# Optimization experiments

Hardware: AMD Instinct MI355X
Metric: run time of the kernel (lower is better)

The kernel has to match this reference:

```python
import jax, jax.numpy as jnp
import numpy as np

N_NODES = 50000
N_EDGES = 800000
N_GRAPHS = 64
IN_DIM, HID_DIM, OUT_DIM = 128, 256, 1


def setup_inputs() -> dict:
    key = jax.random.key(0)
    ks = jax.random.split(key, 9)
    x = jax.random.normal(ks[0], (N_NODES, IN_DIM), dtype=jnp.float32)
    edge_index = jax.random.randint(ks[1], (2, N_EDGES), 0, N_NODES, dtype=jnp.int64)
    batch = jnp.sort(jax.random.randint(ks[2], (N_NODES,), 0, N_GRAPHS, dtype=jnp.int64))
    W1 = jax.random.normal(ks[3], (IN_DIM, HID_DIM), dtype=jnp.float32) / np.sqrt(IN_DIM)
    b1 = jax.random.normal(ks[4], (HID_DIM,), dtype=jnp.float32) * 0.01
    W2 = jax.random.normal(ks[5], (HID_DIM, HID_DIM), dtype=jnp.float32) / np.sqrt(HID_DIM)
    b2 = jax.random.normal(ks[6], (HID_DIM,), dtype=jnp.float32) * 0.01
    Wfc = jax.random.normal(ks[7], (HID_DIM, OUT_DIM), dtype=jnp.float32) / np.sqrt(HID_DIM)
    bfc = jax.random.normal(ks[8], (OUT_DIM,), dtype=jnp.float32) * 0.01
    return {"x": x, "edge_index": edge_index, "batch": batch,
            "W1": W1, "b1": b1, "W2": W2, "b2": b2, "Wfc": Wfc, "bfc": bfc}


def reference(x, edge_index, batch, W1, b1, W2, b2, Wfc, bfc):
    N = x.shape[0]
    loop = jnp.arange(N, dtype=edge_index.dtype)
    src = jnp.concatenate([edge_index[0], loop])  # [E+N] message sources
    dst = jnp.concatenate([edge_index[1], loop])  # [E+N] aggregation targets
    # symmetric GCN normalization with self-loops
    deg = jax.ops.segment_sum(jnp.ones_like(dst, dtype=x.dtype), dst, num_segments=N)
    dinv = jnp.where(deg > 0, jax.lax.rsqrt(deg), 0.0)
    norm = (dinv[src] * dinv[dst])[:, None]  # [E+N, 1]

    def gcn(h, W, b):
        h = h @ W                                     # [N, H]
        msg = h[src] * norm                           # gather + scale
        return jax.ops.segment_sum(msg, dst, num_segments=N) + b

    h = jax.nn.relu(gcn(x, W1, b1))
    h = jax.nn.relu(gcn(h, W2, b2))
    # global mean pool over graphs in the batch
    counts = jax.ops.segment_sum(jnp.ones((N,), dtype=h.dtype), batch, num_segments=N_GRAPHS)
    sums = jax.ops.segment_sum(h, batch, num_segments=N_GRAPHS)
    pooled = sums / jnp.maximum(counts, 1.0)[:, None]  # [G, H]
    out = pooled @ Wfc + bfc                           # [G, 1]
    return out.squeeze(-1)
```

## Files before the change

### kernel.cpp

```cpp
#include <hip/hip_runtime.h>
#include <hip/hip_bf16.h>

#define N_NODES 50000
#define N_EDGES 800000
#define N_GRAPHS 64
#define IN_DIM 128
#define HID_DIM 256
#define M_PAD 50048

typedef short sh8 __attribute__((ext_vector_type(8)));
typedef float f4 __attribute__((ext_vector_type(4)));
typedef float f2 __attribute__((ext_vector_type(2)));
typedef unsigned short us4 __attribute__((ext_vector_type(4)));

__device__ __forceinline__ unsigned short bf16rne(float f) {
    unsigned int u = __float_as_uint(f);
    return (unsigned short)((u + 0x7FFFu + ((u >> 16) & 1u)) >> 16);
}
__device__ __forceinline__ float bf2f(unsigned short b) {
    return __uint_as_float((unsigned int)b << 16);
}
__device__ __forceinline__ unsigned char f32_to_fp8(float v) {
    int p = __builtin_amdgcn_cvt_pk_fp8_f32(v, v, 0, false);
    return (unsigned char)(p & 0xFF);
}

__device__ __forceinline__ void gl2lds16(const unsigned short* g, unsigned short* l) {
    __builtin_amdgcn_global_load_lds(
        (const __attribute__((address_space(1))) void*)g,
        (__attribute__((address_space(3))) void*)l, 16, 0, 0);
}


__device__ __forceinline__ void wconv_one(const float* __restrict__ W,
                                          unsigned short* __restrict__ Bh, int i) {
    int k = i >> 8, c = i & 255;
    size_t pos = (size_t)(k >> 5) * 8192 + (size_t)(((c >> 4) * 4 + ((k >> 3) & 3)) * 128 + (c & 15) * 8 + (k & 7));
    Bh[pos] = bf16rne(W[i]);
}

__global__ __launch_bounds__(256)
void k_prep(const float* __restrict__ W1, unsigned short* __restrict__ Bh1,
            const float* __restrict__ W2, unsigned short* __restrict__ Bh2,
            const int* __restrict__ batch, int* __restrict__ bounds, float* __restrict__ sums,
            const int* __restrict__ dst, int* __restrict__ deg_i) {
    const int T = gridDim.x * 256;
    const int gid = blockIdx.x * 256 + threadIdx.x;
    for (int i = gid; i < IN_DIM * 256; i += T) wconv_one(W1, Bh1, i);
    for (int i = gid; i < HID_DIM * 256; i += T) wconv_one(W2, Bh2, i);
    for (int i = gid; i < N_GRAPHS * HID_DIM; i += T) sums[i] = 0.f;
    if (gid <= N_GRAPHS) {
        int lo = 0, hi = N_NODES;
        while (lo < hi) {
            int mid = (lo + hi) >> 1;
            if (batch[mid] < gid) lo = mid + 1; else hi = mid;
        }
        bounds[gid] = lo;
    }
    for (int e = gid; e < N_EDGES; e += T) atomicAdd(&deg_i[dst[e]], 1);
}

#define SCAN_BLK 1024
#define SCAN_NBLK ((N_NODES + SCAN_BLK - 1) / SCAN_BLK)

__global__ __launch_bounds__(SCAN_BLK)
void k_scan_blk(const int* __restrict__ deg, int* __restrict__ row_start,
                float* __restrict__ dinv, int* __restrict__ blk_tot) {
    __shared__ int tmp[SCAN_BLK];
    int t = threadIdx.x;
    int i = blockIdx.x * SCAN_BLK + t;
    int d = 0;
    if (i < N_NODES) {
        d = deg[i];
        dinv[i] = rsqrtf((float)d + 1.0f);
    }
    tmp[t] = d;
    __syncthreads();
    #pragma unroll
    for (int off = 1; off < SCAN_BLK; off <<= 1) {
        int v = (t >= off) ? tmp[t - off] : 0;
        __syncthreads();
        tmp[t] += v;
        __syncthreads();
    }
    if (i < N_NODES) row_start[i] = tmp[t] - d;
    if (t == SCAN_BLK - 1) blk_tot[blockIdx.x] = tmp[t];
}

__global__ __launch_bounds__(SCAN_BLK)
void k_scan_add(int* __restrict__ row_start, const int* __restrict__ blk_tot) {
    __shared__ int soff;
    int t = threadIdx.x;
    int bid = blockIdx.x;
    if (t < 64) {
        int v = (t < bid) ? blk_tot[t] : 0;
        #pragma unroll
        for (int m = 1; m < 64; m <<= 1) v += __shfl_xor(v, m, 64);
        if (t == 0) soff = v;
    }
    __syncthreads();
    int i = bid * SCAN_BLK + t;
    if (i < N_NODES) row_start[i] += soff;
    if (bid == 0 && t == 0) row_start[N_NODES] = N_EDGES;
}

__global__ __launch_bounds__(256)
void k_x2f8(const float* __restrict__ x, const float* __restrict__ dinv,
            unsigned char* __restrict__ xf8) {
    int i = blockIdx.x * blockDim.x + threadIdx.x;
    if (i >= N_NODES * IN_DIM / 4) return;
    float4 v = ((const float4*)x)[i];
    float s = dinv[i >> 5] * 8.f;
    unsigned int lo = (unsigned int)__builtin_amdgcn_cvt_pk_fp8_f32(v.x * s, v.y * s, 0, false) & 0xFFFFu;
    unsigned int hi = (unsigned int)__builtin_amdgcn_cvt_pk_fp8_f32(v.z * s, v.w * s, 0, false) & 0xFFFFu;
    ((unsigned int*)xf8)[i] = lo | (hi << 16);
}

__global__ void k_csr_fill(const int* __restrict__ src, const int* __restrict__ dst,
                           const int* __restrict__ row_start, int* __restrict__ cursor,
                           int* __restrict__ col) {
    int e = blockIdx.x * blockDim.x + threadIdx.x;
    if (e < N_EDGES) {
        int d = dst[e];
        int pos = atomicAdd(&cursor[d], 1);
        col[row_start[d] + pos] = src[e];
    }
}


template<int MODE>
__global__ __launch_bounds__(256)
void k_gemm_mfma(const unsigned short* __restrict__ Ah,
                 const unsigned short* __restrict__ Bh,
                 const float* __restrict__ dinv, const float* __restrict__ bias,
                 unsigned short* __restrict__ Cbf, unsigned char* __restrict__ Cf8,
                 int M, int K) {
    __shared__ unsigned short AhL[2][2][2048];

    const int tid = threadIdx.x;
    const int wv = tid >> 6, lane = tid & 63;
    const int m0 = blockIdx.x * 64;

    const int ar = wv * 16 + (lane & 15);
    const int kseg = lane >> 4;
    const unsigned short* aph = Ah + (size_t)(m0 + ar) * K + kseg * 8;
    const int adoff = (wv * 64 + lane) * 8;

    f4 acc[4][4];
    #pragma unroll
    for (int mi = 0; mi < 4; ++mi)
        #pragma unroll
        for (int nj = 0; nj < 4; ++nj)
            acc[mi][nj] = f4{0.f, 0.f, 0.f, 0.f};

    const int nsteps = K >> 6;
    gl2lds16(aph, &AhL[0][0][adoff]);
    gl2lds16(aph + 32, &AhL[0][1][adoff]);

    int cur = 0;
    for (int s = 0; s < nsteps; ++s) {
        __syncthreads();
        if (s + 1 < nsteps) {
            gl2lds16(aph + (s + 1) * 64, &AhL[cur ^ 1][0][adoff]);
            gl2lds16(aph + (s + 1) * 64 + 32, &AhL[cur ^ 1][1][adoff]);
        }
        #pragma unroll
        for (int kk = 0; kk < 2; ++kk) {
            const int bstep = s * 2 + kk;
            const unsigned short* gb = Bh + (size_t)bstep * 8192 + wv * 2048 + lane * 8;
            sh8 bfh[4];
            #pragma unroll
            for (int nj = 0; nj < 4; ++nj)
                bfh[nj] = *reinterpret_cast<const sh8*>(gb + nj * 512);
            sh8 afh[4];
            #pragma unroll
            for (int mi = 0; mi < 4; ++mi)
                afh[mi] = *reinterpret_cast<const sh8*>(&AhL[cur][kk][mi * 512 + lane * 8]);
            #pragma unroll
            for (int mi = 0; mi < 4; ++mi)
                #pragma unroll
                for (int nj = 0; nj < 4; ++nj)
                    acc[mi][nj] = __builtin_amdgcn_mfma_f32_16x16x32_bf16(afh[mi], bfh[nj], acc[mi][nj], 0, 0, 0);
        }
        cur ^= 1;
    }

    #pragma unroll
    for (int mi = 0; mi < 4; ++mi) {
        #pragma unroll
        for (int q = 0; q < 4; ++q) {
            int grow = m0 + mi * 16 + (lane >> 4) * 4 + q;
            if (grow < M) {
                float dm16 = (MODE == 0) ? dinv[grow] * 16.f : 0.f;
                #pragma unroll
                for (int nj = 0; nj < 4; ++nj) {
                    int gcol = wv * 64 + nj * 16 + (lane & 15);
                    float v = acc[mi][nj][q];
                    if (MODE == 0) {
                        Cf8[(size_t)grow * 256 + gcol] = f32_to_fp8(v * dm16);
                    } else {
                        Cbf[(size_t)grow * 256 + gcol] = bf16rne(fmaxf(v + bias[gcol], 0.f));
                    }
                }
            }
        }
    }
}


__global__ __launch_bounds__(256)
void k_agg_x(const float* __restrict__ x, const unsigned char* __restrict__ xf8,
             const int* __restrict__ row_start, const int* __restrict__ col,
             const float* __restrict__ dinv, unsigned short* __restrict__ zh) {
    int wv = threadIdx.x >> 6, lane = threadIdx.x & 63;
    int half = lane >> 5, sub = lane & 31;
    int n = blockIdx.x * 4 + wv;

    float a0 = 0.f, a1 = 0.f, a2 = 0.f, a3 = 0.f;
    float dn = dinv[n];
    if (half == 0) {
        float4 xs = ((const float4*)x)[(size_t)n * 32 + sub];
        a0 = xs.x * dn * 8.f; a1 = xs.y * dn * 8.f;
        a2 = xs.z * dn * 8.f; a3 = xs.w * dn * 8.f;
    }
    const unsigned int* xw = (const unsigned int*)xf8;
    int e = row_start[n] + half;
    const int e1 = row_start[n + 1];
    for (; e + 14 < e1; e += 16) {
        int s0 = col[e], s1 = col[e + 2], s2 = col[e + 4], s3 = col[e + 6];
        int s4 = col[e + 8], s5 = col[e + 10], s6 = col[e + 12], s7 = col[e + 14];
        unsigned int w0 = xw[(size_t)s0 * 32 + sub], w1 = xw[(size_t)s1 * 32 + sub];
        unsigned int w2 = xw[(size_t)s2 * 32 + sub], w3 = xw[(size_t)s3 * 32 + sub];
        unsigned int w4 = xw[(size_t)s4 * 32 + sub], w5 = xw[(size_t)s5 * 32 + sub];
        unsigned int w6 = xw[(size_t)s6 * 32 + sub], w7 = xw[(size_t)s7 * 32 + sub];
        #pragma unroll
        for (int k = 0; k < 8; ++k) {
            unsigned int w = (k == 0) ? w0 : (k == 1) ? w1 : (k == 2) ? w2 : (k == 3) ? w3
                           : (k == 4) ? w4 : (k == 5) ? w5 : (k == 6) ? w6 : w7;
            f2 p0 = __builtin_amdgcn_cvt_pk_f32_fp8(w, false);
            f2 p1 = __builtin_amdgcn_cvt_pk_f32_fp8(w, true);
            a0 += p0.x; a1 += p0.y; a2 += p1.x; a3 += p1.y;
        }
    }
    for (; e + 6 < e1; e += 8) {
        int s0 = col[e], s1 = col[e + 2], s2 = col[e + 4], s3 = col[e + 6];
        unsigned int w0 = xw[(size_t)s0 * 32 + sub], w1 = xw[(size_t)s1 * 32 + sub];
        unsigned int w2 = xw[(size_t)s2 * 32 + sub], w3 = xw[(size_t)s3 * 32 + sub];
        #pragma unroll
        for (int k = 0; k < 4; ++k) {
            unsigned int w = (k == 0) ? w0 : (k == 1) ? w1 : (k == 2) ? w2 : w3;
            f2 p0 = __builtin_amdgcn_cvt_pk_f32_fp8(w, false);
            f2 p1 = __builtin_amdgcn_cvt_pk_f32_fp8(w, true);
            a0 += p0.x; a1 += p0.y; a2 += p1.x; a3 += p1.y;
        }
    }
    for (; e < e1; e += 2) {
        int s = col[e];
        unsigned int w = xw[(size_t)s * 32 + sub];
        f2 p0 = __builtin_amdgcn_cvt_pk_f32_fp8(w, false);
        f2 p1 = __builtin_amdgcn_cvt_pk_f32_fp8(w, true);
        a0 += p0.x; a1 += p0.y; a2 += p1.x; a3 += p1.y;
    }
    a0 += __shfl_xor(a0, 32, 64);
    a1 += __shfl_xor(a1, 32, 64);
    a2 += __shfl_xor(a2, 32, 64);
    a3 += __shfl_xor(a3, 32, 64);
    if (half == 0) {
        float s = dn * 0.125f;
        us4 oh;
        oh.x = bf16rne(a0 * s);
        oh.y = bf16rne(a1 * s);
        oh.z = bf16rne(a2 * s);
        oh.w = bf16rne(a3 * s);
        ((us4*)zh)[(size_t)n * 32 + sub] = oh;
    }
}

__global__ __launch_bounds__(512)
void k_agg_pool(const unsigned char* __restrict__ yb, const int* __restrict__ row_start,
                const int* __restrict__ col, const float* __restrict__ dinv,
                const float* __restrict__ bias, const int* __restrict__ batch,
                float* __restrict__ sums) {
    __shared__ float lsum[8][256];
    const int tid = threadIdx.x;
    const int wv = tid >> 6, lane = tid & 63;
    const int half = lane >> 5, sub = lane & 31;
    const int base = blockIdx.x * 8;
    const int n = base + wv;

    const bool uni = (batch[base] == batch[base + 7]);

    const uint2* y8 = (const uint2*)yb;
    float a[8] = {0.f, 0.f, 0.f, 0.f, 0.f, 0.f, 0.f, 0.f};
    if (half == 0) {
        uint2 w = y8[(size_t)n * 32 + sub];
        f2 p0 = __builtin_amdgcn_cvt_pk_f32_fp8(w.x, false);
        f2 p1 = __builtin_amdgcn_cvt_pk_f32_fp8(w.x, true);
        f2 p2 = __builtin_amdgcn_cvt_pk_f32_fp8(w.y, false);
        f2 p3 = __builtin_amdgcn_cvt_pk_f32_fp8(w.y, true);
        a[0] = p0.x; a[1] = p0.y; a[2] = p1.x; a[3] = p1.y;
        a[4] = p2.x; a[5] = p2.y; a[6] = p3.x; a[7] = p3.y;
    }
    int e = row_start[n] + half;
    const int e1 = row_start[n + 1];
    for (; e + 14 < e1; e += 16) {
        int s0 = col[e], s1 = col[e + 2], s2 = col[e + 4], s3 = col[e + 6];
        int s4 = col[e + 8], s5 = col[e + 10], s6 = col[e + 12], s7 = col[e + 14];
        uint2 w0 = y8[(size_t)s0 * 32 + sub], w1 = y8[(size_t)s1 * 32 + sub];
        uint2 w2 = y8[(size_t)s2 * 32 + sub], w3 = y8[(size_t)s3 * 32 + sub];
        uint2 w4 = y8[(size_t)s4 * 32 + sub], w5 = y8[(size_t)s5 * 32 + sub];
        uint2 w6 = y8[(size_t)s6 * 32 + sub], w7 = y8[(size_t)s7 * 32 + sub];
        #pragma unroll
        for (int k = 0; k < 8; ++k) {
            uint2 w = (k == 0) ? w0 : (k == 1) ? w1 : (k == 2) ? w2 : (k == 3) ? w3
                    : (k == 4) ? w4 : (k == 5) ? w5 : (k == 6) ? w6 : w7;
            f2 p0 = __builtin_amdgcn_cvt_pk_f32_fp8(w.x, false);
            f2 p1 = __builtin_amdgcn_cvt_pk_f32_fp8(w.x, true);
            f2 p2 = __builtin_amdgcn_cvt_pk_f32_fp8(w.y, false);
            f2 p3 = __builtin_amdgcn_cvt_pk_f32_fp8(w.y, true);
            a[0] += p0.x; a[1] += p0.y; a[2] += p1.x; a[3] += p1.y;
            a[4] += p2.x; a[5] += p2.y; a[6] += p3.x; a[7] += p3.y;
        }
    }
    for (; e + 6 < e1; e += 8) {
        int s0 = col[e], s1 = col[e + 2], s2 = col[e + 4], s3 = col[e + 6];
        uint2 w0 = y8[(size_t)s0 * 32 + sub], w1 = y8[(size_t)s1 * 32 + sub];
        uint2 w2 = y8[(size_t)s2 * 32 + sub], w3 = y8[(size_t)s3 * 32 + sub];
        #pragma unroll
        for (int k = 0; k < 4; ++k) {
            uint2 w = (k == 0) ? w0 : (k == 1) ? w1 : (k == 2) ? w2 : w3;
            f2 p0 = __builtin_amdgcn_cvt_pk_f32_fp8(w.x, false);
            f2 p1 = __builtin_amdgcn_cvt_pk_f32_fp8(w.x, true);
            f2 p2 = __builtin_amdgcn_cvt_pk_f32_fp8(w.y, false);
            f2 p3 = __builtin_amdgcn_cvt_pk_f32_fp8(w.y, true);
            a[0] += p0.x; a[1] += p0.y; a[2] += p1.x; a[3] += p1.y;
            a[4] += p2.x; a[5] += p2.y; a[6] += p3.x; a[7] += p3.y;
        }
    }
    for (; e < e1; e += 2) {
        int s = col[e];
        uint2 w = y8[(size_t)s * 32 + sub];
        f2 p0 = __builtin_amdgcn_cvt_pk_f32_fp8(w.x, false);
        f2 p1 = __builtin_amdgcn_cvt_pk_f32_fp8(w.x, true);
        f2 p2 = __builtin_amdgcn_cvt_pk_f32_fp8(w.y, false);
        f2 p3 = __builtin_amdgcn_cvt_pk_f32_fp8(w.y, true);
        a[0] += p0.x; a[1] += p0.y; a[2] += p1.x; a[3] += p1.y;
        a[4] += p2.x; a[5] += p2.y; a[6] += p3.x; a[7] += p3.y;
    }
    #pragma unroll
    for (int j = 0; j < 8; ++j) a[j] += __shfl_xor(a[j], 32, 64);

    if (half == 0) {
        float dn = dinv[n] * 0.0625f;
        float4 b0 = ((const float4*)bias)[sub * 2];
        float4 b1 = ((const float4*)bias)[sub * 2 + 1];
        float4 o0, o1;
        o0.x = fmaxf(a[0] * dn + b0.x, 0.f);
        o0.y = fmaxf(a[1] * dn + b0.y, 0.f);
        o0.z = fmaxf(a[2] * dn + b0.z, 0.f);
        o0.w = fmaxf(a[3] * dn + b0.w, 0.f);
        o1.x = fmaxf(a[4] * dn + b1.x, 0.f);
        o1.y = fmaxf(a[5] * dn + b1.y, 0.f);
        o1.z = fmaxf(a[6] * dn + b1.z, 0.f);
        o1.w = fmaxf(a[7] * dn + b1.w, 0.f);
        if (uni) {
            ((float4*)&lsum[wv][sub * 8])[0] = o0;
            ((float4*)&lsum[wv][sub * 8])[1] = o1;
        } else {
            int g = batch[n];
            atomicAdd(&sums[g * 256 + sub * 8 + 0], o0.x);
            atomicAdd(&sums[g * 256 + sub * 8 + 1], o0.y);
            atomicAdd(&sums[g * 256 + sub * 8 + 2], o0.z);
            atomicAdd(&sums[g * 256 + sub * 8 + 3], o0.w);
            atomicAdd(&sums[g * 256 + sub * 8 + 4], o1.x);
            atomicAdd(&sums[g * 256 + sub * 8 + 5], o1.y);
            atomicAdd(&sums[g * 256 + sub * 8 + 6], o1.z);
            atomicAdd(&sums[g * 256 + sub * 8 + 7], o1.w);
        }
    }
    __syncthreads();
    if (uni && tid < 256) {
        float v = 0.f;
        #pragma unroll
        for (int w = 0; w < 8; ++w) v += lsum[w][tid];
        atomicAdd(&sums[batch[base] * 256 + tid], v);
    }
}


__global__ void k_final(const float* __restrict__ sums, const int* __restrict__ bounds,
                        const float* __restrict__ Wfc, const float* __restrict__ bfc,
                        float* __restrict__ out) {
    __shared__ float red[HID_DIM];
    int g = blockIdx.x;
    int c = threadIdx.x;
    float cnt = (float)(bounds[g + 1] - bounds[g]);
    float v = sums[g * HID_DIM + c] / fmaxf(cnt, 1.0f) * Wfc[c];
    red[c] = v;
    __syncthreads();
    for (int s = HID_DIM / 2; s > 0; s >>= 1) {
        if (c < s) red[c] += red[c + s];
        __syncthreads();
    }
    if (c == 0) out[g] = red[0] + bfc[0];
}


extern "C" void kernel_launch(void* const* d_in, const int* in_sizes, int n_in,
                              void* d_out, int out_size, void* d_ws, size_t ws_size,
                              hipStream_t stream) {
    const float* x    = (const float*)d_in[0];
    const int*   ei   = (const int*)d_in[1];
    const int*   batch= (const int*)d_in[2];
    const float* W1   = (const float*)d_in[3];
    const float* b1   = (const float*)d_in[4];
    const float* W2   = (const float*)d_in[5];
    const float* b2   = (const float*)d_in[6];
    const float* Wfc  = (const float*)d_in[7];
    const float* bfc  = (const float*)d_in[8];
    float* out = (float*)d_out;

    const int* src = ei;
    const int* dst = ei + N_EDGES;

    char* ws = (char*)d_ws;
    const size_t PLANE256 = (size_t)M_PAD * 256 * 2;
    size_t off = 0;
    unsigned short* h1h = (unsigned short*)(ws + off); off += PLANE256;
    char*           r1  = (char*)(ws + off); off += PLANE256;
    unsigned char*  xf8 = (unsigned char*)(ws + off); off += (size_t)N_NODES * 128;
    int*   deg_i     = (int*)  (ws + off); off += 200704;
    int*   cursor    = (int*)  (ws + off); off += 200704;
    float* dinv      = (float*)(ws + off); off += 200704;
    int*   row_start = (int*)  (ws + off); off += 200704;
    int*   col       = (int*)  (ws + off); off += (size_t)N_EDGES * 4;
    unsigned short* Bh1 = (unsigned short*)(ws + off); off += 65536;
    unsigned short* Bh2 = (unsigned short*)(ws + off); off += 131072;
    float* sums      = (float*)(ws + off); off += 65536;
    int*   bounds    = (int*)  (ws + off); off += 512;
    int*   blk_tot   = (int*)  (ws + off); off += 512;
    (void)ws_size; (void)in_sizes; (void)n_in; (void)out_size;

    unsigned short* zh   = (unsigned short*)r1;
    unsigned char*  y2f8 = (unsigned char*)r1;

    hipMemsetAsync(deg_i, 0, 2 * 200704, stream);
    k_prep<<<2048, 256, 0, stream>>>(W1, Bh1, W2, Bh2, batch, bounds, sums, dst, deg_i);
    k_scan_blk<<<SCAN_NBLK, SCAN_BLK, 0, stream>>>(deg_i, row_start, dinv, blk_tot);
    k_scan_add<<<SCAN_NBLK, SCAN_BLK, 0, stream>>>(row_start, blk_tot);
    k_x2f8<<<(N_NODES * IN_DIM / 4 + 255) / 256, 256, 0, stream>>>(x, dinv, xf8);
    k_csr_fill<<<(N_EDGES + 255) / 256, 256, 0, stream>>>(src, dst, row_start, cursor, col);

    const int gemm_grid = (N_NODES + 63) / 64;

    k_agg_x<<<N_NODES / 4, 256, 0, stream>>>(x, xf8, row_start, col, dinv, zh);
    k_gemm_mfma<1><<<gemm_grid, 256, 0, stream>>>(zh, Bh1, dinv, b1, h1h, nullptr, N_NODES, IN_DIM);

    k_gemm_mfma<0><<<gemm_grid, 256, 0, stream>>>(h1h, Bh2, dinv, b2, nullptr, y2f8, N_NODES, HID_DIM);
    k_agg_pool<<<N_NODES / 8, 512, 0, stream>>>(y2f8, row_start, col, dinv, b2, batch, sums);

    k_final<<<N_GRAPHS, HID_DIM, 0, stream>>>(sums, bounds, Wfc, bfc, out);
}
```

Baseline: 221.6 us.

## Fuse scan-fix with fp8 cast, fold final reduction into pool, specialize GEMM K

Merges the scan offset fix and the x-to-fp8 conversion into one grid-stride kernel. The final per-graph reduction moves into the tail of the aggregation/pool kernel through a last-block atomic counter. The GEMM is templated on K, and the K=128 case loads the whole A tile at once with a single barrier. The 16-wide unrolled gather loop is also removed from agg_pool. These cut launch overhead and barrier stalls, at the cost of a serialized tail done by one block and a dependence on the sync counter being zeroed by the existing memset.

After: 355.9 us. +60.6%, slower.

```diff
diff --git a/kernel.cpp b/kernel.cpp
--- a/kernel.cpp
+++ b/kernel.cpp
@@ -88,32 +88,31 @@
 }
 
 __global__ __launch_bounds__(SCAN_BLK)
-void k_scan_add(int* __restrict__ row_start, const int* __restrict__ blk_tot) {
-    __shared__ int soff;
-    int t = threadIdx.x;
-    int bid = blockIdx.x;
-    if (t < 64) {
-        int v = (t < bid) ? blk_tot[t] : 0;
-        #pragma unroll
-        for (int m = 1; m < 64; m <<= 1) v += __shfl_xor(v, m, 64);
-        if (t == 0) soff = v;
-    }
-    __syncthreads();
-    int i = bid * SCAN_BLK + t;
-    if (i < N_NODES) row_start[i] += soff;
-    if (bid == 0 && t == 0) row_start[N_NODES] = N_EDGES;
-}
-
-__global__ __launch_bounds__(256)
-void k_x2f8(const float* __restrict__ x, const float* __restrict__ dinv,
-            unsigned char* __restrict__ xf8) {
-    int i = blockIdx.x * blockDim.x + threadIdx.x;
-    if (i >= N_NODES * IN_DIM / 4) return;
-    float4 v = ((const float4*)x)[i];
-    float s = dinv[i >> 5] * 8.f;
-    unsigned int lo = (unsigned int)__builtin_amdgcn_cvt_pk_fp8_f32(v.x * s, v.y * s, 0, false) & 0xFFFFu;
-    unsigned int hi = (unsigned int)__builtin_amdgcn_cvt_pk_fp8_f32(v.z * s, v.w * s, 0, false) & 0xFFFFu;
-    ((unsigned int*)xf8)[i] = lo | (hi << 16);
+void k_scan_fix(int* __restrict__ row_start, const int* __restrict__ blk_tot,
+                const float* __restrict__ x, const float* __restrict__ dinv,
+                unsigned char* __restrict__ xf8) {
+    const int t = threadIdx.x, bid = blockIdx.x;
+    if (bid < SCAN_NBLK) {
+        __shared__ int soff;
+        if (t < 64) {
+            int v = (t < bid) ? blk_tot[t] : 0;
+            #pragma unroll
+            for (int m = 1; m < 64; m <<= 1) v += __shfl_xor(v, m, 64);
+            if (t == 0) soff = v;
+        }
+        __syncthreads();
+        int i = bid * SCAN_BLK + t;
+        if (i < N_NODES) row_start[i] += soff;
+        if (bid == 0 && t == 0) row_start[N_NODES] = N_EDGES;
+    }
+    const int T = gridDim.x * SCAN_BLK;
+    for (int i = bid * SCAN_BLK + t; i < N_NODES * IN_DIM / 4; i += T) {
+        float4 v = ((const float4*)x)[i];
+        float s = dinv[i >> 5] * 8.f;
+        unsigned int lo = (unsigned int)__builtin_amdgcn_cvt_pk_fp8_f32(v.x * s, v.y * s, 0, false) & 0xFFFFu;
+        unsigned int hi = (unsigned int)__builtin_amdgcn_cvt_pk_fp8_f32(v.z * s, v.w * s, 0, false) & 0xFFFFu;
+        ((unsigned int*)xf8)[i] = lo | (hi << 16);
+    }
 }
 
 __global__ void k_csr_fill(const int* __restrict__ src, const int* __restrict__ dst,
@@ -128,14 +127,14 @@
 }
 
 
-template<int MODE>
+template<int MODE, int K>
 __global__ __launch_bounds__(256)
 void k_gemm_mfma(const unsigned short* __restrict__ Ah,
                  const unsigned short* __restrict__ Bh,
                  const float* __restrict__ dinv, const float* __restrict__ bias,
                  unsigned short* __restrict__ Cbf, unsigned char* __restrict__ Cf8,
-                 int M, int K) {
-    __shared__ unsigned short AhL[2][2][2048];
+                 int M) {
+    __shared__ unsigned short AhL[4][2048];
 
     const int tid = threadIdx.x;
     const int wv = tid >> 6, lane = tid & 63;
@@ -153,21 +152,13 @@
         for (int nj = 0; nj < 4; ++nj)
             acc[mi][nj] = f4{0.f, 0.f, 0.f, 0.f};
 
-    const int nsteps = K >> 6;
-    gl2lds16(aph, &AhL[0][0][adoff]);
-    gl2lds16(aph + 32, &AhL[0][1][adoff]);
-
-    int cur = 0;
-    for (int s = 0; s < nsteps; ++s) {
+    if constexpr (K == 128) {
+        #pragma unroll
+        for (int c = 0; c < 4; ++c) gl2lds16(aph + c * 32, &AhL[c][adoff]);
         __syncthreads();
-        if (s + 1 < nsteps) {
-            gl2lds16(aph + (s + 1) * 64, &AhL[cur ^ 1][0][adoff]);
-            gl2lds16(aph + (s + 1) * 64 + 32, &AhL[cur ^ 1][1][adoff]);
-        }
-        #pragma unroll
-        for (int kk = 0; kk < 2; ++kk) {
-            const int bstep = s * 2 + kk;
-            const unsigned short* gb = Bh + (size_t)bstep * 8192 + wv * 2048 + lane * 8;
+        #pragma unroll
+        for (int kk = 0; kk < 4; ++kk) {
+            const unsigned short* gb = Bh + (size_t)kk * 8192 + wv * 2048 + lane * 8;
             sh8 bfh[4];
             #pragma unroll
             for (int nj = 0; nj < 4; ++nj)
@@ -175,14 +166,44 @@
             sh8 afh[4];
             #pragma unroll
             for (int mi = 0; mi < 4; ++mi)
-                afh[mi] = *reinterpret_cast<const sh8*>(&AhL[cur][kk][mi * 512 + lane * 8]);
+                afh[mi] = *reinterpret_cast<const sh8*>(&AhL[kk][mi * 512 + lane * 8]);
             #pragma unroll
             for (int mi = 0; mi < 4; ++mi)
                 #pragma unroll
                 for (int nj = 0; nj < 4; ++nj)
                     acc[mi][nj] = __builtin_amdgcn_mfma_f32_16x16x32_bf16(afh[mi], bfh[nj], acc[mi][nj], 0, 0, 0);
         }
-        cur ^= 1;
+    } else {
+        const int nsteps = K >> 6;
+        gl2lds16(aph, &AhL[0][adoff]);
+        gl2lds16(aph + 32, &AhL[1][adoff]);
+        int cur = 0;
+        for (int s = 0; s < nsteps; ++s) {
+            __syncthreads();
+            if (s + 1 < nsteps) {
+                gl2lds16(aph + (s + 1) * 64, &AhL[(cur ^ 1) * 2][adoff]);
+                gl2lds16(aph + (s + 1) * 64 + 32, &AhL[(cur ^ 1) * 2 + 1][adoff]);
+            }
+            #pragma unroll
+            for (int kk = 0; kk < 2; ++kk) {
+                const int bstep = s * 2 + kk;
+                const unsigned short* gb = Bh + (size_t)bstep * 8192 + wv * 2048 + lane * 8;
+                sh8 bfh[4];
+                #pragma unroll
+                for (int nj = 0; nj < 4; ++nj)
+                    bfh[nj] = *reinterpret_cast<const sh8*>(gb + nj * 512);
+                sh8 afh[4];
+                #pragma unroll
+                for (int mi = 0; mi < 4; ++mi)
+                    afh[mi] = *reinterpret_cast<const sh8*>(&AhL[cur * 2 + kk][mi * 512 + lane * 8]);
+                #pragma unroll
+                for (int mi = 0; mi < 4; ++mi)
+                    #pragma unroll
+                    for (int nj = 0; nj < 4; ++nj)
+                        acc[mi][nj] = __builtin_amdgcn_mfma_f32_16x16x32_bf16(afh[mi], bfh[nj], acc[mi][nj], 0, 0, 0);
+            }
+            cur ^= 1;
+        }
     }
 
     #pragma unroll
@@ -280,8 +301,11 @@
 void k_agg_pool(const unsigned char* __restrict__ yb, const int* __restrict__ row_start,
                 const int* __restrict__ col, const float* __restrict__ dinv,
                 const float* __restrict__ bias, const int* __restrict__ batch,
-                float* __restrict__ sums) {
+                float* __restrict__ sums, unsigned int* __restrict__ sync_cnt,
+                const int* __restrict__ bounds, const float* __restrict__ Wfc,
+                const float* __restrict__ bfc, float* __restrict__ out) {
     __shared__ float lsum[8][256];
+    __shared__ bool doneS;
     const int tid = threadIdx.x;
     const int wv = tid >> 6, lane = tid & 63;
     const int half = lane >> 5, sub = lane & 31;
@@ -303,25 +327,6 @@
     }
     int e = row_start[n] + half;
     const int e1 = row_start[n + 1];
-    for (; e + 14 < e1; e += 16) {
-        int s0 = col[e], s1 = col[e + 2], s2 = col[e + 4], s3 = col[e + 6];
-        int s4 = col[e + 8], s5 = col[e + 10], s6 = col[e + 12], s7 = col[e + 14];
-        uint2 w0 = y8[(size_t)s0 * 32 + sub], w1 = y8[(size_t)s1 * 32 + sub];
-        uint2 w2 = y8[(size_t)s2 * 32 + sub], w3 = y8[(size_t)s3 * 32 + sub];
-        uint2 w4 = y8[(size_t)s4 * 32 + sub], w5 = y8[(size_t)s5 * 32 + sub];
-        uint2 w6 = y8[(size_t)s6 * 32 + sub], w7 = y8[(size_t)s7 * 32 + sub];
-        #pragma unroll
-        for (int k = 0; k < 8; ++k) {
-            uint2 w = (k == 0) ? w0 : (k == 1) ? w1 : (k == 2) ? w2 : (k == 3) ? w3
-                    : (k == 4) ? w4 : (k == 5) ? w5 : (k == 6) ? w6 : w7;
-            f2 p0 = __builtin_amdgcn_cvt_pk_f32_fp8(w.x, false);
-            f2 p1 = __builtin_amdgcn_cvt_pk_f32_fp8(w.x, true);
-            f2 p2 = __builtin_amdgcn_cvt_pk_f32_fp8(w.y, false);
-            f2 p3 = __builtin_amdgcn_cvt_pk_f32_fp8(w.y, true);
-            a[0] += p0.x; a[1] += p0.y; a[2] += p1.x; a[3] += p1.y;
-            a[4] += p2.x; a[5] += p2.y; a[6] += p3.x; a[7] += p3.y;
-        }
-    }
     for (; e + 6 < e1; e += 8) {
         int s0 = col[e], s1 = col[e + 2], s2 = col[e + 4], s3 = col[e + 6];
         uint2 w0 = y8[(size_t)s0 * 32 + sub], w1 = y8[(size_t)s1 * 32 + sub];
@@ -385,24 +390,29 @@
         for (int w = 0; w < 8; ++w) v += lsum[w][tid];
         atomicAdd(&sums[batch[base] * 256 + tid], v);
     }
-}
-
-
-__global__ void k_final(const float* __restrict__ sums, const int* __restrict__ bounds,
-                        const float* __restrict__ Wfc, const float* __restrict__ bfc,
-                        float* __restrict__ out) {
-    __shared__ float red[HID_DIM];
-    int g = blockIdx.x;
-    int c = threadIdx.x;
-    float cnt = (float)(bounds[g + 1] - bounds[g]);
-    float v = sums[g * HID_DIM + c] / fmaxf(cnt, 1.0f) * Wfc[c];
-    red[c] = v;
+
     __syncthreads();
-    for (int s = HID_DIM / 2; s > 0; s >>= 1) {
-        if (c < s) red[c] += red[c + s];
-        __syncthreads();
-    }
-    if (c == 0) out[g] = red[0] + bfc[0];
+    if (tid == 0) {
+        __threadfence();
+        unsigned int t = atomicAdd(sync_cnt, 1u);
+        doneS = (t == (unsigned int)(gridDim.x - 1));
+    }
+    __syncthreads();
+    if (doneS) {
+        __threadfence();
+        int w = tid >> 6, ln = tid & 63;
+        #pragma unroll
+        for (int gi = 0; gi < 8; ++gi) {
+            int g = w * 8 + gi;
+            float cnt = (float)(bounds[g + 1] - bounds[g]);
+            float v = 0.f;
+            #pragma unroll
+            for (int c = 0; c < 4; ++c) v += sums[g * 256 + ln + c * 64] * Wfc[ln + c * 64];
+            #pragma unroll
+            for (int m = 1; m < 64; m <<= 1) v += __shfl_xor(v, m, 64);
+            if (ln == 0) out[g] = v / fmaxf(cnt, 1.f) + bfc[0];
+        }
+    }
 }
 
 
@@ -443,21 +453,20 @@
 
     unsigned short* zh   = (unsigned short*)r1;
     unsigned char*  y2f8 = (unsigned char*)r1;
+    unsigned int* sync_cnt = (unsigned int*)(cursor + N_NODES);
 
     hipMemsetAsync(deg_i, 0, 2 * 200704, stream);
     k_prep<<<2048, 256, 0, stream>>>(W1, Bh1, W2, Bh2, batch, bounds, sums, dst, deg_i);
     k_scan_blk<<<SCAN_NBLK, SCAN_BLK, 0, stream>>>(deg_i, row_start, dinv, blk_tot);
-    k_scan_add<<<SCAN_NBLK, SCAN_BLK, 0, stream>>>(row_start, blk_tot);
-    k_x2f8<<<(N_NODES * IN_DIM / 4 + 255) / 256, 256, 0, stream>>>(x, dinv, xf8);
+    k_scan_fix<<<256, SCAN_BLK, 0, stream>>>(row_start, blk_tot, x, dinv, xf8);
     k_csr_fill<<<(N_EDGES + 255) / 256, 256, 0, stream>>>(src, dst, row_start, cursor, col);
 
     const int gemm_grid = (N_NODES + 63) / 64;
 
     k_agg_x<<<N_NODES / 4, 256, 0, stream>>>(x, xf8, row_start, col, dinv, zh);
-    k_gemm_mfma<1><<<gemm_grid, 256, 0, stream>>>(zh, Bh1, dinv, b1, h1h, nullptr, N_NODES, IN_DIM);
-
-    k_gemm_mfma<0><<<gemm_grid, 256, 0, stream>>>(h1h, Bh2, dinv, b2, nullptr, y2f8, N_NODES, HID_DIM);
-    k_agg_pool<<<N_NODES / 8, 512, 0, stream>>>(y2f8, row_start, col, dinv, b2, batch, sums);
-
-    k_final<<<N_GRAPHS, HID_DIM, 0, stream>>>(sums, bounds, Wfc, bfc, out);
-}
+    k_gemm_mfma<1, 128><<<gemm_grid, 256, 0, stream>>>(zh, Bh1, dinv, b1, h1h, nullptr, N_NODES);
+
+    k_gemm_mfma<0, 256><<<gemm_grid, 256, 0, stream>>>(h1h, Bh2, dinv, b2, nullptr, y2f8, N_NODES);
+    k_agg_pool<<<N_NODES / 8, 512, 0, stream>>>(y2f8, row_start, col, dinv, b2, batch,
+                                                sums, sync_cnt, bounds, Wfc, bfc, out);
+}
```
